# Kernel tuning notes

Hardware: AMD Instinct MI355X
Metric: run time of the kernel (lower is better)

The kernel has to match this reference:

```python
import jax, jax.numpy as jnp
import numpy as np

N = 100000
E = 3200000
D_IN = 256
D_OUT = 256
K = 3


def setup_inputs() -> dict:
    key = jax.random.key(0)
    k1, k2, k3, k4, k5 = jax.random.split(key, 5)
    x = jax.random.normal(k1, (N, D_IN), dtype=jnp.float32)
    # xavier-uniform-ish weight
    lim = float(np.sqrt(6.0 / (D_IN + D_OUT)))
    weight = jax.random.uniform(k2, (D_IN, D_OUT), dtype=jnp.float32, minval=-lim, maxval=lim)
    bias = jnp.zeros((D_OUT,), dtype=jnp.float32)
    edge_weight = jax.random.uniform(k3, (E,), dtype=jnp.float32) / 32.0  # ~normalized adj values
    edge_row = jax.random.randint(k4, (E,), 0, N, dtype=jnp.int32)
    edge_col = jax.random.randint(k5, (E,), 0, N, dtype=jnp.int32)
    return {"x": x, "weight": weight, "bias": bias, "edge_weight": edge_weight,
            "edge_row": edge_row, "edge_col": edge_col}


def _spmm(edge_weight, edge_row, edge_col, support):
    # out[i] = sum_{e: row_e == i} w_e * support[col_e]
    msgs = edge_weight[:, None] * support[edge_col]  # [E, D]
    return jax.ops.segment_sum(msgs, edge_row, num_segments=N)


def reference(x, weight, bias, edge_weight, edge_row, edge_col):
    support = x @ weight            # [N, D_OUT]
    output = support
    for _ in range(K):
        support = _spmm(edge_weight, edge_row, edge_col, support)
        output = output + support
    return output + bias
```

## Files before the change

kernel.cpp:

```cpp
#include <hip/hip_runtime.h>

#define D 256
#define NB 196
#define RPB_SHIFT 9
#define CAP 20480
#define CHUNK 8192
#define PADSLACK 4096

typedef __attribute__((ext_vector_type(8))) short bf16x8;
typedef __attribute__((ext_vector_type(4))) float f32x4;
typedef __attribute__((ext_vector_type(2))) float f32x2;

__device__ __forceinline__ unsigned bf16rne(float f) {
    unsigned u = __float_as_uint(f);
    return (u + 0x7fffu + ((u >> 16) & 1u)) >> 16;
}
__device__ __forceinline__ unsigned char fp8enc(float f) {
    return (unsigned char)(__builtin_amdgcn_cvt_pk_fp8_f32(f, f, 0, false) & 0xFF);
}


__global__ __launch_bounds__(256) void cursor_init(int* __restrict__ g) {
    int t = threadIdx.x;
    g[t] = t * CAP;
}

__global__ __launch_bounds__(256) void partA(const int* __restrict__ erow,
                                             const int* __restrict__ ecol,
                                             const float* __restrict__ ew,
                                             int* __restrict__ gcur,
                                             int2* __restrict__ temp, int E) {
    __shared__ int2 rec[CHUNK];
    __shared__ unsigned char bkt[CHUNK];
    __shared__ int hist[256], sc[256], excl[256], cur[256], lbase[256];
    int t = threadIdx.x;
    int base = blockIdx.x * CHUNK;
    hist[t] = 0;
    __syncthreads();
    int rows[32];
    #pragma unroll
    for (int j = 0; j < 32; j++) {
        int e = base + t + 256 * j;
        rows[j] = (e < E) ? erow[e] : -1;
        if (rows[j] >= 0) atomicAdd(&hist[rows[j] >> RPB_SHIFT], 1);
    }
    __syncthreads();
    sc[t] = hist[t];
    __syncthreads();
    for (int off = 1; off < 256; off <<= 1) {
        int v = (t >= off) ? sc[t - off] : 0;
        __syncthreads();
        sc[t] += v;
        __syncthreads();
    }
    int ex = sc[t] - hist[t];
    excl[t] = ex;
    cur[t] = ex;
    lbase[t] = atomicAdd(&gcur[t], hist[t]);
    __syncthreads();
    int total = sc[255];
    #pragma unroll
    for (int j = 0; j < 32; j++) {
        if (rows[j] >= 0) {
            int e = base + t + 256 * j;
            int b = rows[j] >> RPB_SHIFT;
            int rl = rows[j] & 511;
            int p = atomicAdd(&cur[b], 1);
            int2 r;
            r.x = ecol[e] | (rl << 17);
            r.y = __float_as_int(ew[e]);
            rec[p] = r;
            bkt[p] = (unsigned char)b;
        }
    }
    __syncthreads();
    for (int i = t; i < total; i += 256) {
        int b = bkt[i];
        temp[(size_t)lbase[b] + (i - excl[b])] = rec[i];
    }
}

__global__ __launch_bounds__(256) void scanB(const int* __restrict__ gcur,
                                             int* __restrict__ bbase) {
    __shared__ int sc[256];
    int t = threadIdx.x;
    int c = (t < NB) ? (gcur[t] - t * CAP) : 0;
    sc[t] = c;
    __syncthreads();
    for (int off = 1; off < 256; off <<= 1) {
        int v = (t >= off) ? sc[t - off] : 0;
        __syncthreads();
        sc[t] += v;
        __syncthreads();
    }
    if (t < NB) bbase[t] = sc[t] - c;
}

__global__ __launch_bounds__(256) void partB(const int2* __restrict__ temp,
                                             const int* __restrict__ gcur,
                                             const int* __restrict__ bbase,
                                             int* __restrict__ rps,
                                             int* __restrict__ rpe,
                                             int2* __restrict__ edges,
                                             int N, int E) {
    __shared__ int hist[512], excl[512], pst[512], scp[256];
    int b = blockIdx.x;
    int t = threadIdx.x;
    int cnt = gcur[b] - b * CAP;
    int base = bbase[b] + b * PADSLACK;
    const int2* src = temp + (size_t)b * CAP;
    hist[t] = 0;
    hist[t + 256] = 0;
    __syncthreads();
    for (int i = t; i < cnt; i += 256)
        atomicAdd(&hist[(src[i].x >> 17) & 511], 1);
    __syncthreads();
    int v0 = hist[2 * t], v1 = hist[2 * t + 1];
    int p0 = (v0 + 7) & ~7, p1 = (v1 + 7) & ~7;
    int ps = p0 + p1;
    scp[t] = ps;
    __syncthreads();
    for (int off = 1; off < 256; off <<= 1) {
        int v = (t >= off) ? scp[t - off] : 0;
        __syncthreads();
        scp[t] += v;
        __syncthreads();
    }
    int ep = scp[t] - ps;
    excl[2 * t] = ep;
    excl[2 * t + 1] = ep + p0;
    pst[2 * t] = ep;
    pst[2 * t + 1] = ep + p0;
    int r0 = (b << RPB_SHIFT) + 2 * t;
    if (r0 < N)     { rps[r0]     = base + ep;      rpe[r0]     = base + ep + p0; }
    if (r0 + 1 < N) { rps[r0 + 1] = base + ep + p0; rpe[r0 + 1] = base + ep + p0 + p1; }
    __syncthreads();
    for (int i = t; i < cnt; i += 256) {
        int2 r = src[i];
        int rl = (r.x >> 17) & 511;
        int p = base + atomicAdd(&excl[rl], 1);
        int2 o;
        o.x = (r.x & 0x1FFFF) << 8;
        o.y = r.y;
        edges[p] = o;
    }
    __syncthreads();
    int c0 = hist[2 * t];
    int b0 = base + pst[2 * t];
    for (int k = c0; k < p0; k++) edges[b0 + k] = make_int2(0, 0);
    int c1 = hist[2 * t + 1];
    int b1 = base + pst[2 * t + 1];
    for (int k = c1; k < p1; k++) edges[b1 + k] = make_int2(0, 0);
}

__global__ __launch_bounds__(256) void wconv_kernel(const float* __restrict__ w,
                                                    bf16x8* __restrict__ Wf) {
    int idx = blockIdx.x * 256 + threadIdx.x;
    int lane = idx & 63, g = idx >> 6;
    int h = g >> 6, r = g & 63;
    int ct = r >> 2, ks = (h << 2) | (r & 3);
    int q = lane >> 4, c = lane & 15;
    int n = ct * 16 + c;
    int k0 = ks * 32 + q * 8;
    bf16x8 bv;
    #pragma unroll
    for (int j = 0; j < 8; j++)
        bv[j] = (short)bf16rne(w[(size_t)(k0 + j) * D + n]);
    Wf[idx] = bv;
}

__global__ __launch_bounds__(512, 4) void gemm_kernel(const float* __restrict__ x,
                                                      const bf16x8* __restrict__ Wf,
                                                      const float* __restrict__ bias,
                                                      unsigned char* __restrict__ s0f8,
                                                      float* __restrict__ out, int N) {
    __shared__ bf16x8 Wl[4096];
    int t = threadIdx.x;
    int wid = t >> 6, lane = t & 63;
    int q = lane >> 4, c = lane & 15;
    int row0 = blockIdx.x * 128 + wid * 16;
    int rA = row0 + c;
    if (rA >= N) rA = N - 1;
    const float* xr = x + (size_t)rA * D + q * 8;

    f32x4 acc[16];
    #pragma unroll
    for (int ct = 0; ct < 16; ct++) acc[ct] = (f32x4){0.f, 0.f, 0.f, 0.f};

    for (int h = 0; h < 2; h++) {
        if (h) __syncthreads();
        #pragma unroll
        for (int k2 = 0; k2 < 8; k2++)
            Wl[k2 * 512 + t] = Wf[h * 4096 + k2 * 512 + t];
        __syncthreads();
        #pragma unroll
        for (int ks2 = 0; ks2 < 4; ks2++) {
            int ks = h * 4 + ks2;
            float4 p = *(const float4*)(xr + ks * 32);
            float4 r = *(const float4*)(xr + ks * 32 + 4);
            bf16x8 a;
            a[0] = (short)bf16rne(p.x); a[1] = (short)bf16rne(p.y);
            a[2] = (short)bf16rne(p.z); a[3] = (short)bf16rne(p.w);
            a[4] = (short)bf16rne(r.x); a[5] = (short)bf16rne(r.y);
            a[6] = (short)bf16rne(r.z); a[7] = (short)bf16rne(r.w);
            #pragma unroll
            for (int ct = 0; ct < 16; ct++) {
                bf16x8 bfrag = Wl[(ct * 4 + ks2) * 64 + lane];
                acc[ct] = __builtin_amdgcn_mfma_f32_16x16x32_bf16(a, bfrag, acc[ct], 0, 0, 0);
            }
        }
    }

    int rbase = row0 + q * 4;
    #pragma unroll
    for (int ct = 0; ct < 16; ct++) {
        int col = ct * 16 + c;
        float bv = bias[col];
        #pragma unroll
        for (int r = 0; r < 4; r++) {
            int rr = rbase + r;
            if (rr < N) {
                float v = acc[ct][r];
                size_t o = (size_t)rr * D + col;
                s0f8[o] = fp8enc(v);
                out[o] = v + bv;
            }
        }
    }
}

__global__ __launch_bounds__(256, 8) void spmm_kernel(const uint2* __restrict__ S2,
                                                      const int* __restrict__ rps,
                                                      const int* __restrict__ rpe,
                                                      const int2* __restrict__ edges,
                                                      uint2* __restrict__ Snext2, int N) {
    int wid = threadIdx.x >> 6;
    int lane = threadIdx.x & 63;
    int half = lane >> 5;
    int hl = lane & 31;
    int rowbase = (blockIdx.x * 4 + wid) * 2;
    if (rowbase >= N) return;
    int row = rowbase + half;
    bool rv = row < N;
    int e   = rv ? rps[row] : 0;
    int end = rv ? rpe[row] : 0;
    const char* Sb = (const char*)S2 + (hl << 3);

    f32x2 acc0 = {0.f, 0.f}, acc1 = {0.f, 0.f}, acc2 = {0.f, 0.f}, acc3 = {0.f, 0.f};

    int2 edn[8];
    #pragma unroll
    for (int j = 0; j < 8; j++) edn[j] = edges[e + j];

    while (e < end) {
        uint2 v[8];
        #pragma unroll
        for (int j = 0; j < 8; j++)
            v[j] = *(const uint2*)(Sb + (unsigned)edn[j].x);
        float w[8];
        #pragma unroll
        for (int j = 0; j < 8; j++) w[j] = __int_as_float(edn[j].y);
        #pragma unroll
        for (int j = 0; j < 8; j++) edn[j] = edges[e + 8 + j];
        #pragma unroll
        for (int j = 0; j < 8; j++) {
            f32x2 w2 = {w[j], w[j]};
            f32x2 l0 = __builtin_amdgcn_cvt_pk_f32_fp8(v[j].x, false);
            f32x2 h0 = __builtin_amdgcn_cvt_pk_f32_fp8(v[j].x, true);
            f32x2 l1 = __builtin_amdgcn_cvt_pk_f32_fp8(v[j].y, false);
            f32x2 h1 = __builtin_amdgcn_cvt_pk_f32_fp8(v[j].y, true);
            acc0 += w2 * l0;
            acc1 += w2 * h0;
            acc2 += w2 * l1;
            acc3 += w2 * h1;
        }
        e += 8;
    }
    if (rv) {
        unsigned s0 = (unsigned)__builtin_amdgcn_cvt_pk_fp8_f32(acc0.x, acc0.y, 0, false);
        s0 = (unsigned)__builtin_amdgcn_cvt_pk_fp8_f32(acc1.x, acc1.y, (int)s0, true);
        unsigned s1 = (unsigned)__builtin_amdgcn_cvt_pk_fp8_f32(acc2.x, acc2.y, 0, false);
        s1 = (unsigned)__builtin_amdgcn_cvt_pk_fp8_f32(acc3.x, acc3.y, (int)s1, true);
        uint2 o; o.x = s0; o.y = s1;
        Snext2[(size_t)row * 32 + hl] = o;
    }
}

__global__ __launch_bounds__(256) void combine_kernel(float4* __restrict__ out,
                                                      const unsigned int* __restrict__ S1,
                                                      const unsigned int* __restrict__ S2,
                                                      const unsigned int* __restrict__ S3,
                                                      int n4) {
    int i = blockIdx.x * 256 + threadIdx.x;
    if (i >= n4) return;
    unsigned u1 = S1[i], u2 = S2[i], u3 = S3[i];
    f32x2 l1 = __builtin_amdgcn_cvt_pk_f32_fp8(u1, false);
    f32x2 h1 = __builtin_amdgcn_cvt_pk_f32_fp8(u1, true);
    f32x2 l2 = __builtin_amdgcn_cvt_pk_f32_fp8(u2, false);
    f32x2 h2 = __builtin_amdgcn_cvt_pk_f32_fp8(u2, true);
    f32x2 l3 = __builtin_amdgcn_cvt_pk_f32_fp8(u3, false);
    f32x2 h3 = __builtin_amdgcn_cvt_pk_f32_fp8(u3, true);
    float4 o = out[i];
    o.x += l1.x + l2.x + l3.x;
    o.y += l1.y + l2.y + l3.y;
    o.z += h1.x + h2.x + h3.x;
    o.w += h1.y + h2.y + h3.y;
    out[i] = o;
}

extern "C" void kernel_launch(void* const* d_in, const int* in_sizes, int n_in,
                              void* d_out, int out_size, void* d_ws, size_t ws_size,
                              hipStream_t stream) {
    const float* x      = (const float*)d_in[0];
    const float* weight = (const float*)d_in[1];
    const float* bias   = (const float*)d_in[2];
    const float* ew     = (const float*)d_in[3];
    const int*   erow   = (const int*)d_in[4];
    const int*   ecol   = (const int*)d_in[5];
    float* out = (float*)d_out;
    int N = in_sizes[0] / D;
    int E = in_sizes[3];

    char* ws = (char*)d_ws;
    size_t off = 0;
    auto walloc = [&](size_t bytes) -> void* {
        void* p = ws + off;
        off += (bytes + 255) & ~255ULL;
        return p;
    };
    unsigned char* Sa = (unsigned char*)walloc((size_t)N * D);
    unsigned char* Sb = (unsigned char*)walloc((size_t)N * D);
    unsigned char* Sc = (unsigned char*)walloc((size_t)N * D);
    int*    rps     = (int*)walloc((size_t)N * 4);
    int*    rpe     = (int*)walloc((size_t)N * 4);
    int*    gcur    = (int*)walloc(256 * 4);
    int*    bbase   = (int*)walloc(256 * 4);
    bf16x8* Wf      = (bf16x8*)walloc(128 * 64 * 16);
    int2*   temp    = (int2*)walloc((size_t)NB * CAP * 8);
    int2*   edges   = (int2*)walloc(((size_t)E + (size_t)NB * PADSLACK + 64) * 8);

    cursor_init<<<1, 256, 0, stream>>>(gcur);
    int nchunks = (E + CHUNK - 1) / CHUNK;
    partA<<<nchunks, 256, 0, stream>>>(erow, ecol, ew, gcur, temp, E);
    scanB<<<1, 256, 0, stream>>>(gcur, bbase);
    partB<<<NB, 256, 0, stream>>>(temp, gcur, bbase, rps, rpe, edges, N, E);

    wconv_kernel<<<32, 256, 0, stream>>>(weight, Wf);
    gemm_kernel<<<(N + 127) / 128, 512, 0, stream>>>(x, Wf, bias, Sa, out, N);

    int sb = (N + 7) / 8;
    spmm_kernel<<<sb, 256, 0, stream>>>((const uint2*)Sa, rps, rpe, edges,
                                        (uint2*)Sb, N);
    spmm_kernel<<<sb, 256, 0, stream>>>((const uint2*)Sb, rps, rpe, edges,
                                        (uint2*)Sc, N);
    spmm_kernel<<<sb, 256, 0, stream>>>((const uint2*)Sc, rps, rpe, edges,
                                        (uint2*)Sa, N);

    int n4 = N * (D / 4);
    combine_kernel<<<(n4 + 255) / 256, 256, 0, stream>>>((float4*)out,
                                                         (const unsigned int*)Sb,
                                                         (const unsigned int*)Sc,
                                                         (const unsigned int*)Sa, n4);
}
```

Baseline: 700.7 us.

## Widen SpMM gathers to 16-byte loads and fuse the final combine into the last SpMM

```diff
diff --git a/kernel.cpp b/kernel.cpp
--- a/kernel.cpp
+++ b/kernel.cpp
@@ -229,34 +229,33 @@
     }
 }
 
-__global__ __launch_bounds__(256, 8) void spmm_kernel(const uint2* __restrict__ S2,
+__global__ __launch_bounds__(256, 4) void spmm_kernel(const unsigned char* __restrict__ S,
                                                       const int* __restrict__ rps,
                                                       const int* __restrict__ rpe,
                                                       const int2* __restrict__ edges,
-                                                      uint2* __restrict__ Snext2, int N) {
-    int wid = threadIdx.x >> 6;
-    int lane = threadIdx.x & 63;
-    int half = lane >> 5;
-    int hl = lane & 31;
-    int rowbase = (blockIdx.x * 4 + wid) * 2;
-    if (rowbase >= N) return;
-    int row = rowbase + half;
-    bool rv = row < N;
-    int e   = rv ? rps[row] : 0;
-    int end = rv ? rpe[row] : 0;
-    const char* Sb = (const char*)S2 + (hl << 3);
-
-    f32x2 acc0 = {0.f, 0.f}, acc1 = {0.f, 0.f}, acc2 = {0.f, 0.f}, acc3 = {0.f, 0.f};
+                                                      unsigned char* __restrict__ Snext, int N) {
+    int t = threadIdx.x;
+    int wid = t >> 6, lane = t & 63;
+    int q = lane >> 4, ql = lane & 15;
+    int row = blockIdx.x * 16 + wid * 4 + q;
+    if (row >= N) return;
+    int e   = rps[row];
+    int end = rpe[row];
+    const unsigned char* Sl = S + (ql << 4);
+
+    f32x2 A[8];
+    #pragma unroll
+    for (int i = 0; i < 8; i++) A[i] = (f32x2){0.f, 0.f};
 
     int2 edn[8];
     #pragma unroll
     for (int j = 0; j < 8; j++) edn[j] = edges[e + j];
 
     while (e < end) {
-        uint2 v[8];
+        uint4 v[8];
         #pragma unroll
         for (int j = 0; j < 8; j++)
-            v[j] = *(const uint2*)(Sb + (unsigned)edn[j].x);
+            v[j] = *(const uint4*)(Sl + (unsigned)edn[j].x);
         float w[8];
         #pragma unroll
         for (int j = 0; j < 8; j++) w[j] = __int_as_float(edn[j].y);
@@ -265,47 +264,98 @@
         #pragma unroll
         for (int j = 0; j < 8; j++) {
             f32x2 w2 = {w[j], w[j]};
-            f32x2 l0 = __builtin_amdgcn_cvt_pk_f32_fp8(v[j].x, false);
-            f32x2 h0 = __builtin_amdgcn_cvt_pk_f32_fp8(v[j].x, true);
-            f32x2 l1 = __builtin_amdgcn_cvt_pk_f32_fp8(v[j].y, false);
-            f32x2 h1 = __builtin_amdgcn_cvt_pk_f32_fp8(v[j].y, true);
-            acc0 += w2 * l0;
-            acc1 += w2 * h0;
-            acc2 += w2 * l1;
-            acc3 += w2 * h1;
+            A[0] += w2 * __builtin_amdgcn_cvt_pk_f32_fp8(v[j].x, false);
+            A[1] += w2 * __builtin_amdgcn_cvt_pk_f32_fp8(v[j].x, true);
+            A[2] += w2 * __builtin_amdgcn_cvt_pk_f32_fp8(v[j].y, false);
+            A[3] += w2 * __builtin_amdgcn_cvt_pk_f32_fp8(v[j].y, true);
+            A[4] += w2 * __builtin_amdgcn_cvt_pk_f32_fp8(v[j].z, false);
+            A[5] += w2 * __builtin_amdgcn_cvt_pk_f32_fp8(v[j].z, true);
+            A[6] += w2 * __builtin_amdgcn_cvt_pk_f32_fp8(v[j].w, false);
+            A[7] += w2 * __builtin_amdgcn_cvt_pk_f32_fp8(v[j].w, true);
         }
         e += 8;
     }
-    if (rv) {
-        unsigned s0 = (unsigned)__builtin_amdgcn_cvt_pk_fp8_f32(acc0.x, acc0.y, 0, false);
-        s0 = (unsigned)__builtin_amdgcn_cvt_pk_fp8_f32(acc1.x, acc1.y, (int)s0, true);
-        unsigned s1 = (unsigned)__builtin_amdgcn_cvt_pk_fp8_f32(acc2.x, acc2.y, 0, false);
-        s1 = (unsigned)__builtin_amdgcn_cvt_pk_fp8_f32(acc3.x, acc3.y, (int)s1, true);
-        uint2 o; o.x = s0; o.y = s1;
-        Snext2[(size_t)row * 32 + hl] = o;
-    }
-}
-
-__global__ __launch_bounds__(256) void combine_kernel(float4* __restrict__ out,
-                                                      const unsigned int* __restrict__ S1,
-                                                      const unsigned int* __restrict__ S2,
-                                                      const unsigned int* __restrict__ S3,
-                                                      int n4) {
-    int i = blockIdx.x * 256 + threadIdx.x;
-    if (i >= n4) return;
-    unsigned u1 = S1[i], u2 = S2[i], u3 = S3[i];
-    f32x2 l1 = __builtin_amdgcn_cvt_pk_f32_fp8(u1, false);
-    f32x2 h1 = __builtin_amdgcn_cvt_pk_f32_fp8(u1, true);
-    f32x2 l2 = __builtin_amdgcn_cvt_pk_f32_fp8(u2, false);
-    f32x2 h2 = __builtin_amdgcn_cvt_pk_f32_fp8(u2, true);
-    f32x2 l3 = __builtin_amdgcn_cvt_pk_f32_fp8(u3, false);
-    f32x2 h3 = __builtin_amdgcn_cvt_pk_f32_fp8(u3, true);
-    float4 o = out[i];
-    o.x += l1.x + l2.x + l3.x;
-    o.y += l1.y + l2.y + l3.y;
-    o.z += h1.x + h2.x + h3.x;
-    o.w += h1.y + h2.y + h3.y;
-    out[i] = o;
+    unsigned s;
+    uint4 o;
+    s   = (unsigned)__builtin_amdgcn_cvt_pk_fp8_f32(A[0].x, A[0].y, 0, false);
+    o.x = (unsigned)__builtin_amdgcn_cvt_pk_fp8_f32(A[1].x, A[1].y, (int)s, true);
+    s   = (unsigned)__builtin_amdgcn_cvt_pk_fp8_f32(A[2].x, A[2].y, 0, false);
+    o.y = (unsigned)__builtin_amdgcn_cvt_pk_fp8_f32(A[3].x, A[3].y, (int)s, true);
+    s   = (unsigned)__builtin_amdgcn_cvt_pk_fp8_f32(A[4].x, A[4].y, 0, false);
+    o.z = (unsigned)__builtin_amdgcn_cvt_pk_fp8_f32(A[5].x, A[5].y, (int)s, true);
+    s   = (unsigned)__builtin_amdgcn_cvt_pk_fp8_f32(A[6].x, A[6].y, 0, false);
+    o.w = (unsigned)__builtin_amdgcn_cvt_pk_fp8_f32(A[7].x, A[7].y, (int)s, true);
+    *(uint4*)(Snext + (size_t)row * 256 + (ql << 4)) = o;
+}
+
+__global__ __launch_bounds__(256, 4) void spmm_fused_kernel(const unsigned char* __restrict__ S,
+                                                            const int* __restrict__ rps,
+                                                            const int* __restrict__ rpe,
+                                                            const int2* __restrict__ edges,
+                                                            const unsigned char* __restrict__ S1,
+                                                            float* __restrict__ out, int N) {
+    int t = threadIdx.x;
+    int wid = t >> 6, lane = t & 63;
+    int q = lane >> 4, ql = lane & 15;
+    int row = blockIdx.x * 16 + wid * 4 + q;
+    if (row >= N) return;
+    int e   = rps[row];
+    int end = rpe[row];
+    const unsigned char* Sl = S + (ql << 4);
+
+    f32x2 A[8];
+    #pragma unroll
+    for (int i = 0; i < 8; i++) A[i] = (f32x2){0.f, 0.f};
+
+    int2 edn[8];
+    #pragma unroll
+    for (int j = 0; j < 8; j++) edn[j] = edges[e + j];
+
+    while (e < end) {
+        uint4 v[8];
+        #pragma unroll
+        for (int j = 0; j < 8; j++)
+            v[j] = *(const uint4*)(Sl + (unsigned)edn[j].x);
+        float w[8];
+        #pragma unroll
+        for (int j = 0; j < 8; j++) w[j] = __int_as_float(edn[j].y);
+        #pragma unroll
+        for (int j = 0; j < 8; j++) edn[j] = edges[e + 8 + j];
+        #pragma unroll
+        for (int j = 0; j < 8; j++) {
+            f32x2 w2 = {w[j], w[j]};
+            A[0] += w2 * __builtin_amdgcn_cvt_pk_f32_fp8(v[j].x, false);
+            A[1] += w2 * __builtin_amdgcn_cvt_pk_f32_fp8(v[j].x, true);
+            A[2] += w2 * __builtin_amdgcn_cvt_pk_f32_fp8(v[j].y, false);
+            A[3] += w2 * __builtin_amdgcn_cvt_pk_f32_fp8(v[j].y, true);
+            A[4] += w2 * __builtin_amdgcn_cvt_pk_f32_fp8(v[j].z, false);
+            A[5] += w2 * __builtin_amdgcn_cvt_pk_f32_fp8(v[j].z, true);
+            A[6] += w2 * __builtin_amdgcn_cvt_pk_f32_fp8(v[j].w, false);
+            A[7] += w2 * __builtin_amdgcn_cvt_pk_f32_fp8(v[j].w, true);
+        }
+        e += 8;
+    }
+    size_t rb = (size_t)row * 256 + (ql << 4);
+    uint4 u1 = *(const uint4*)(S1 + rb);
+    uint4 u2 = *(const uint4*)(S + rb);
+    A[0] += __builtin_amdgcn_cvt_pk_f32_fp8(u1.x, false) + __builtin_amdgcn_cvt_pk_f32_fp8(u2.x, false);
+    A[1] += __builtin_amdgcn_cvt_pk_f32_fp8(u1.x, true)  + __builtin_amdgcn_cvt_pk_f32_fp8(u2.x, true);
+    A[2] += __builtin_amdgcn_cvt_pk_f32_fp8(u1.y, false) + __builtin_amdgcn_cvt_pk_f32_fp8(u2.y, false);
+    A[3] += __builtin_amdgcn_cvt_pk_f32_fp8(u1.y, true)  + __builtin_amdgcn_cvt_pk_f32_fp8(u2.y, true);
+    A[4] += __builtin_amdgcn_cvt_pk_f32_fp8(u1.z, false) + __builtin_amdgcn_cvt_pk_f32_fp8(u2.z, false);
+    A[5] += __builtin_amdgcn_cvt_pk_f32_fp8(u1.z, true)  + __builtin_amdgcn_cvt_pk_f32_fp8(u2.z, true);
+    A[6] += __builtin_amdgcn_cvt_pk_f32_fp8(u1.w, false) + __builtin_amdgcn_cvt_pk_f32_fp8(u2.w, false);
+    A[7] += __builtin_amdgcn_cvt_pk_f32_fp8(u1.w, true)  + __builtin_amdgcn_cvt_pk_f32_fp8(u2.w, true);
+    float* op = out + (size_t)row * 256 + (ql << 4);
+    #pragma unroll
+    for (int k = 0; k < 4; k++) {
+        float4 o = *(const float4*)(op + 4 * k);
+        o.x += A[2 * k].x;
+        o.y += A[2 * k].y;
+        o.z += A[2 * k + 1].x;
+        o.w += A[2 * k + 1].y;
+        *(float4*)(op + 4 * k) = o;
+    }
 }
 
 extern "C" void kernel_launch(void* const* d_in, const int* in_sizes, int n_in,
@@ -348,17 +398,8 @@
     wconv_kernel<<<32, 256, 0, stream>>>(weight, Wf);
     gemm_kernel<<<(N + 127) / 128, 512, 0, stream>>>(x, Wf, bias, Sa, out, N);
 
-    int sb = (N + 7) / 8;
-    spmm_kernel<<<sb, 256, 0, stream>>>((const uint2*)Sa, rps, rpe, edges,
-                                        (uint2*)Sb, N);
-    spmm_kernel<<<sb, 256, 0, stream>>>((const uint2*)Sb, rps, rpe, edges,
-                                        (uint2*)Sc, N);
-    spmm_kernel<<<sb, 256, 0, stream>>>((const uint2*)Sc, rps, rpe, edges,
-                                        (uint2*)Sa, N);
-
-    int n4 = N * (D / 4);
-    combine_kernel<<<(n4 + 255) / 256, 256, 0, stream>>>((float4*)out,
-                                                         (const unsigned int*)Sb,
-                                                         (const unsigned int*)Sc,
-                                                         (const unsigned int*)Sa, n4);
-}
+    int sb = (N + 15) / 16;
+    spmm_kernel<<<sb, 256, 0, stream>>>(Sa, rps, rpe, edges, Sb, N);
+    spmm_kernel<<<sb, 256, 0, stream>>>(Sb, rps, rpe, edges, Sc, N);
+    spmm_fused_kernel<<<sb, 256, 0, stream>>>(Sc, rps, rpe, edges, Sb, out, N);
+}
```

Result: no change. 694.8 us (-0.8%).
